# Optimization experiments

Measured on AMD Instinct MI355X. Metric: run time of the kernel, lower is better.

## Reference

```python
import jax, jax.numpy as jnp
import numpy as np

B, S, D, H = 2, 2048, 1024, 16
DK = D // H
ROPE_BASE = 10000.0


def setup_inputs() -> dict:
    key = jax.random.key(0)
    ks = jax.random.split(key, 6)
    x = jax.random.normal(ks[0], (B, S, D), dtype=jnp.float32)
    # causal mask, broadcastable to [B,H,S,S]; masked_fill where mask==0
    mask = jnp.tril(jnp.ones((S, S), dtype=bool))[None, None]
    position_ids = jnp.tile(jnp.arange(S, dtype=jnp.int32)[None, :], (B, 1))
    sc = 1.0 / np.sqrt(D)
    Wq = jax.random.normal(ks[1], (D, D), dtype=jnp.float32) * sc
    Wk = jax.random.normal(ks[2], (D, D), dtype=jnp.float32) * sc
    Wv = jax.random.normal(ks[3], (D, D), dtype=jnp.float32) * sc
    Wo = jax.random.normal(ks[4], (D, D), dtype=jnp.float32) * sc
    bo = jnp.zeros((D,), dtype=jnp.float32)
    return {"x": x, "mask": mask, "position_ids": position_ids,
            "Wq": Wq, "Wk": Wk, "Wv": Wv, "Wo": Wo, "bo": bo}


def _rotate_half(t):
    t1, t2 = t[..., : t.shape[-1] // 2], t[..., t.shape[-1] // 2:]
    return jnp.concatenate((-t2, t1), axis=-1)


def reference(x, mask, position_ids, Wq, Wk, Wv, Wo, bo):
    b, s, d = x.shape
    h, dk = H, DK
    scale = 1.0 / np.sqrt(dk)

    def proj(W):  # torch Linear: x @ W.T -> [b,h,s,dk]
        return (x @ W.T).reshape(b, s, h, dk).transpose(0, 2, 1, 3)

    Q, K, V = proj(Wq), proj(Wk), proj(Wv)

    # rotary tables (computed in fp32, matching RotaryEmbedding)
    inv_freq = 1.0 / (ROPE_BASE ** (jnp.arange(0, dk, 2, dtype=jnp.float32) / dk))
    t = jnp.arange(s, dtype=jnp.float32)
    freqs = jnp.outer(t, inv_freq)            # [s, dk/2]
    emb = jnp.concatenate((freqs, freqs), -1) # [s, dk]
    cos = jnp.cos(emb)[position_ids][:, None]  # [b,1,s,dk]
    sin = jnp.sin(emb)[position_ids][:, None]
    Q = Q * cos + _rotate_half(Q) * sin
    K = K * cos + _rotate_half(K) * sin

    scores = jnp.einsum('bhqd,bhkd->bhqk', Q, K) * scale
    scores = jnp.where(mask, scores, jnp.float32(-1e9))
    attn = jax.nn.softmax(scores, axis=-1)  # dropout is identity in eval
    out = jnp.einsum('bhqk,bhkd->bhqd', attn, V)
    out = out.transpose(0, 2, 1, 3).reshape(b, s, d)
    return out @ Wo.T + bo
```

## Files before the change

### kernel.cpp

```cpp
#include <hip/hip_runtime.h>
#include <hip/hip_bf16.h>
#include <cstdint>

#define BB 2
#define SS 2048
#define DD 1024
#define HH 16
#define DK 64
#define MROWS (BB*SS)
#define NQKV  (3*DD)

typedef __bf16 bf16x8 __attribute__((ext_vector_type(8)));
typedef float  f32x4  __attribute__((ext_vector_type(4)));
typedef float  f32x16 __attribute__((ext_vector_type(16)));
typedef unsigned u32x2 __attribute__((ext_vector_type(2)));

static __device__ __forceinline__ unsigned short f2bf(float f) {
    __bf16 h = (__bf16)f;
    return __builtin_bit_cast(unsigned short, h);
}
static __device__ __forceinline__ float bf2f(unsigned short u) {
    return (float)__builtin_bit_cast(__bf16, u);
}

#define GLOAD16(gsrc, ldst) \
    __builtin_amdgcn_global_load_lds((const __attribute__((address_space(1))) void*)(gsrc), \
                                     (__attribute__((address_space(3))) void*)(ldst), 16, 0, 0)

static __device__ __forceinline__ void pl32_swap(unsigned &x, unsigned &y) {
#if __has_builtin(__builtin_amdgcn_permlane32_swap)
    u32x2 r = __builtin_amdgcn_permlane32_swap(x, y, false, false);
    x = r[0]; y = r[1];
#else
    asm volatile("v_permlane32_swap_b32 %0, %1" : "+v"(x), "+v"(y));
#endif
}
static __device__ __forceinline__ float swap_half(float v, bool hi) {
    unsigned x = __builtin_bit_cast(unsigned, v), y = x;
    pl32_swap(x, y);
    return __builtin_bit_cast(float, hi ? x : y);
}
template<int BASE> static __device__ __forceinline__ bf16x8 cvt_chunk(const f32x16 &p) {
    unsigned x0, y0, x1, y1;
    asm("v_cvt_pk_bf16_f32 %0, %1, %2" : "=v"(x0) : "v"(p[BASE+0]), "v"(p[BASE+1]));
    asm("v_cvt_pk_bf16_f32 %0, %1, %2" : "=v"(y0) : "v"(p[BASE+4]), "v"(p[BASE+5]));
    asm("v_cvt_pk_bf16_f32 %0, %1, %2" : "=v"(x1) : "v"(p[BASE+2]), "v"(p[BASE+3]));
    asm("v_cvt_pk_bf16_f32 %0, %1, %2" : "=v"(y1) : "v"(p[BASE+6]), "v"(p[BASE+7]));
    pl32_swap(x0, y0);
    pl32_swap(x1, y1);
    union { unsigned u[4]; bf16x8 v; } r;
    r.u[0] = x0; r.u[1] = x1; r.u[2] = y0; r.u[3] = y1;
    return r.v;
}

__global__ void cast_all(const float* __restrict__ x,  const float* __restrict__ wq,
                         const float* __restrict__ wk, const float* __restrict__ wv,
                         const float* __restrict__ wo,
                         unsigned short* __restrict__ xb, unsigned short* __restrict__ wqkv,
                         unsigned short* __restrict__ wob)
{
    const int NX = MROWS * DD;
    const int NW = DD * DD;
    const int total = (NX + 4 * NW) / 8;
    for (int i = blockIdx.x * blockDim.x + threadIdx.x; i < total; i += gridDim.x * blockDim.x) {
        int base = i * 8;
        const float* src; unsigned short* dst; int off;
        if      (base < NX)          { src = x;  dst = xb;          off = base; }
        else if (base < NX + NW)     { src = wq; dst = wqkv;        off = base - NX; }
        else if (base < NX + 2*NW)   { src = wk; dst = wqkv + NW;   off = base - NX - NW; }
        else if (base < NX + 3*NW)   { src = wv; dst = wqkv + 2*NW; off = base - NX - 2*NW; }
        else                         { src = wo; dst = wob;         off = base - NX - 3*NW; }
        float4 a = *(const float4*)(src + off);
        float4 b = *(const float4*)(src + off + 4);
        union { unsigned short s[8]; uint4 v; } u;
        u.s[0] = f2bf(a.x); u.s[1] = f2bf(a.y); u.s[2] = f2bf(a.z); u.s[3] = f2bf(a.w);
        u.s[4] = f2bf(b.x); u.s[5] = f2bf(b.y); u.s[6] = f2bf(b.z); u.s[7] = f2bf(b.w);
        *(uint4*)(dst + off) = u.v;
    }
}

__global__ void rope_table(float* __restrict__ tabc, float* __restrict__ tabs)
{
    int i = blockIdx.x * blockDim.x + threadIdx.x;
    int s = i >> 5, d = i & 31;
    float inv = exp2f(-(float)d * (13.287712379549449f / 32.f));
    float ang = (float)s * inv;
    tabc[i] = cosf(ang);
    tabs[i] = sinf(ang);
}

__global__ __launch_bounds__(512) void gemm_qkv(
    const unsigned short* __restrict__ A, const unsigned short* __restrict__ Bm,
    const int* __restrict__ pids,
    const float* __restrict__ tabc, const float* __restrict__ tabs,
    unsigned short* __restrict__ Qb, unsigned short* __restrict__ Kb,
    unsigned short* __restrict__ Vr)
{
    __shared__ __align__(16) unsigned short sA[2][16384];
    __shared__ __align__(16) unsigned short sB[2][16384];
    const int tid = threadIdx.x;
    const int w = tid >> 6, l = tid & 63;
    const int wm = w >> 2, wn = w & 3;
    const int lr = l & 15, lg = l >> 4;
    const int swz = (blockIdx.x & 7) * 24 + (blockIdx.x >> 3);
    const int bx = swz % 12, by = swz / 12;
    const int mBase = by * 256;
    const int sr  = tid >> 3;
    const int scb = (tid & 7) * 8;
    const int sksw = scb ^ ((sr & 7) * 8);
    const int rdsw = (lr & 7) * 8;

    f32x4 acc[8][4] = {};

    auto stage = [&](int kt, int bb) {
        #pragma unroll
        for (int r = 0; r < 4; ++r) {
            GLOAD16(A  + (size_t)(mBase + r*64 + sr) * DD + kt + sksw,
                    &sA[bb][r*4096 + sr*64 + scb]);
            GLOAD16(Bm + (size_t)(bx*256 + r*64 + sr) * DD + kt + sksw,
                    &sB[bb][r*4096 + sr*64 + scb]);
        }
    };

    stage(0, 0);
    __syncthreads();

    for (int t = 0; t < 16; ++t) {
        const int cur = t & 1;
        #pragma unroll
        for (int p = 0; p < 4; ++p) {
            const int rh = p & 1, ks = p >> 1;
            bf16x8 af[4], bfv[4];
            #pragma unroll
            for (int rf = 0; rf < 4; ++rf) {
                int ra = wm*128 + rh*64 + rf*16 + lr;
                af[rf] = *(const bf16x8*)&sA[cur][ra*64 + ((ks*32 + lg*8) ^ rdsw)];
            }
            #pragma unroll
            for (int cf = 0; cf < 4; ++cf) {
                int rb = wn*64 + cf*16 + lr;
                bfv[cf] = *(const bf16x8*)&sB[cur][rb*64 + ((ks*32 + lg*8) ^ rdsw)];
            }
            if (p == 0 && t < 15) stage((t+1)*64, cur ^ 1);
            __builtin_amdgcn_s_barrier();
            asm volatile("s_waitcnt lgkmcnt(0)" ::: "memory");
            __builtin_amdgcn_sched_barrier(0);
            __builtin_amdgcn_s_setprio(1);
            #pragma unroll
            for (int rf = 0; rf < 4; ++rf)
                #pragma unroll
                for (int cf = 0; cf < 4; ++cf)
                    acc[rh*4+rf][cf] = __builtin_amdgcn_mfma_f32_16x16x32_bf16(
                        af[rf], bfv[cf], acc[rh*4+rf][cf], 0, 0, 0);
            __builtin_amdgcn_s_setprio(0);
            if (p < 3) __builtin_amdgcn_s_barrier();
        }
        __syncthreads();
    }

    if (bx < 8) {
        const bool isQ = bx < 4;
        unsigned short* dst = isQ ? Qb : Kb;
        const float qsc = isQ ? 0.1803368801111244f : 1.0f;
        const int colbase = (bx & 3)*256 + wn*64;
        #pragma unroll
        for (int rr = 0; rr < 8; ++rr) {
            #pragma unroll
            for (int j = 0; j < 4; ++j) {
                int row = mBase + wm*128 + rr*16 + lg*4 + j;
                int pos = pids[row];
                #pragma unroll
                for (int cf = 0; cf < 2; ++cf) {
                    int d = cf*16 + lr;
                    float cc = tabc[pos*32 + d];
                    float sn = tabs[pos*32 + d];
                    float a  = acc[rr][cf][j];
                    float bb2 = acc[rr][cf+2][j];
                    dst[(size_t)row * DD + colbase + d]      = f2bf((a*cc - bb2*sn) * qsc);
                    dst[(size_t)row * DD + colbase + d + 32] = f2bf((bb2*cc + a*sn) * qsc);
                }
            }
        }
    } else {
        const int colbase = (bx - 8)*256 + wn*64;
        #pragma unroll
        for (int rr = 0; rr < 8; ++rr) {
            #pragma unroll
            for (int j = 0; j < 4; ++j) {
                int row = mBase + wm*128 + rr*16 + lg*4 + j;
                #pragma unroll
                for (int cf = 0; cf < 4; ++cf)
                    Vr[(size_t)row * DD + colbase + cf*16 + lr] = f2bf(acc[rr][cf][j]);
            }
        }
    }
}

__global__ __launch_bounds__(256) void gemm_bt(
    const unsigned short* __restrict__ A, const unsigned short* __restrict__ Bm,
    float* __restrict__ Cout, const float* __restrict__ bias,
    int M, int N, int K)
{
    __shared__ __align__(16) unsigned short sA[2][128 * 64];
    __shared__ __align__(16) unsigned short sB[2][128 * 64];
    const int tid = threadIdx.x;
    const int w = tid >> 6, l = tid & 63;
    const int wm = w >> 1, wn = w & 1;
    const int lr = l & 15, lg = l >> 4;
    const int nwg = gridDim.x;
    const int cpx = nwg >> 3;
    const int swz = (blockIdx.x & 7) * cpx + (blockIdx.x >> 3);
    const int nbx = N >> 7;
    const int bx = swz % nbx, by = swz / nbx;
    const int mBase = by * 128, nBase = bx * 128;
    const int srow = tid >> 3;
    const int skof = (tid & 7) * 8;

    f32x4 acc[4][4] = {};

    #pragma unroll
    for (int i = 0; i < 4; ++i) {
        GLOAD16(A  + (size_t)(mBase + i*32 + srow) * K + skof, &sA[0][i*2048 + w*512]);
        GLOAD16(Bm + (size_t)(nBase + i*32 + srow) * K + skof, &sB[0][i*2048 + w*512]);
    }
    int cur = 0;

    for (int kt = 0; kt < K; kt += 64) {
        __syncthreads();
        if (kt + 64 < K) {
            #pragma unroll
            for (int i = 0; i < 4; ++i) {
                GLOAD16(A  + (size_t)(mBase + i*32 + srow) * K + kt + 64 + skof, &sA[cur^1][i*2048 + w*512]);
                GLOAD16(Bm + (size_t)(nBase + i*32 + srow) * K + kt + 64 + skof, &sB[cur^1][i*2048 + w*512]);
            }
        }
        #pragma unroll
        for (int kk = 0; kk < 2; ++kk) {
            bf16x8 af[4], bfv[4];
            #pragma unroll
            for (int mi = 0; mi < 4; ++mi)
                af[mi] = *(const bf16x8*)&sA[cur][(wm*64 + mi*16 + lr)*64 + kk*32 + lg*8];
            #pragma unroll
            for (int ni = 0; ni < 4; ++ni)
                bfv[ni] = *(const bf16x8*)&sB[cur][(wn*64 + ni*16 + lr)*64 + kk*32 + lg*8];
            #pragma unroll
            for (int mi = 0; mi < 4; ++mi)
                #pragma unroll
                for (int ni = 0; ni < 4; ++ni)
                    acc[mi][ni] = __builtin_amdgcn_mfma_f32_16x16x32_bf16(af[mi], bfv[ni], acc[mi][ni], 0, 0, 0);
        }
        cur ^= 1;
    }
    #pragma unroll
    for (int mi = 0; mi < 4; ++mi) {
        #pragma unroll
        for (int j = 0; j < 4; ++j) {
            int row = mBase + wm*64 + mi*16 + lg*4 + j;
            #pragma unroll
            for (int ni = 0; ni < 4; ++ni) {
                int col = nBase + wn*64 + ni*16 + lr;
                Cout[(size_t)row * N + col] = acc[mi][ni][j] + bias[col];
            }
        }
    }
}

__global__ __launch_bounds__(256) void v_transpose(
    const unsigned short* __restrict__ Vr, unsigned short* __restrict__ Vt)
{
    __shared__ __align__(16) unsigned short sT[64 * 64];
    const int bh = blockIdx.y;
    const int st = blockIdx.x;
    const int b = bh >> 4, h = bh & 15;
    const int tid = threadIdx.x;
    #pragma unroll
    for (int i = 0; i < 2; ++i) {
        int c = tid + i*256;
        int s = c >> 3, cb = c & 7;
        const unsigned short* src = Vr + (size_t)(b*SS + st*64 + s) * DD + h*64 + cb*8;
        uint4 v = *(const uint4*)src;
        *(uint4*)&sT[s*64 + ((cb ^ (s >> 3)) * 8)] = v;
    }
    __syncthreads();
    #pragma unroll
    for (int i = 0; i < 2; ++i) {
        int c = tid + i*256;
        int d = c >> 3, sb = c & 7;
        union { unsigned short u[8]; uint4 v; } o;
        #pragma unroll
        for (int e = 0; e < 8; ++e) {
            int s = sb*8 + e;
            o.u[e] = sT[s*64 + (((d >> 3) ^ (s >> 3)) * 8) + (d & 7)];
        }
        *(uint4*)(Vt + (size_t)(bh*64 + d) * SS + st*64 + sb*8) = o.v;
    }
}

__global__ __launch_bounds__(256, 2) void attn_fwd(
    const unsigned short* __restrict__ Qb,
    const unsigned short* __restrict__ Kb,
    const unsigned short* __restrict__ Vt,
    unsigned short* __restrict__ Ob)
{
    __shared__ __align__(16) unsigned short sK[2][64 * 64];
    __shared__ __align__(16) unsigned short sV[2][64 * 64];
    const int tid = threadIdx.x;
    const int w = tid >> 6, l = tid & 63;
    const int lq = l & 31;
    const int hi5 = l >> 5;
    const bool hb = hi5 != 0;

    const int xcd  = blockIdx.x & 7;
    const int c    = blockIdx.x >> 3;
    const int gsel = c & 3;
    const int t    = c >> 2;
    const int qt   = (t < 8) ? t : 23 - t;
    const int bh   = xcd * 4 + gsel;
    const int b = bh >> 4, h = bh & 15;

    const int srow = tid >> 3;
    const int skof = (tid & 7) * 8;
    const int sksw = skof ^ ((srow & 7) * 8);
    const int sw   = (lq & 7) * 8;
    const float THR = 12.0f;

    const unsigned kR0 = (unsigned)((b*SS + srow) * DD + h*64 + sksw);
    const unsigned kR1 = kR0 + (unsigned)(32 * DD);
    const unsigned vR0 = (unsigned)((bh*64 + srow) * SS + sksw);
    const unsigned vR1 = vR0 + (unsigned)(32 * SS);

    bf16x8 qf[4];
    {
        const unsigned short* qp = Qb + (size_t)(b*SS + qt*128 + w*32 + lq) * DD + h*64 + hi5*8;
        #pragma unroll
        for (int dkc = 0; dkc < 4; ++dkc)
            qf[dkc] = *(const bf16x8*)(qp + dkc*16);
    }
    const int q_lane = qt*128 + w*32 + lq;
    const int wbase  = qt*128 + w*32;
    const int total  = 2*qt + 2;

    f32x16 o0 = {}, o1 = {};
    float mrow = -3.0e38f, lsum = 0.f;
    int cur = 0;

    GLOAD16(Kb + kR0, &sK[0][w*512]);
    GLOAD16(Kb + kR1, &sK[0][2048 + w*512]);
    GLOAD16(Vt + vR0, &sV[0][w*512]);
    GLOAD16(Vt + vR1, &sV[0][2048 + w*512]);

    for (int kt = 0; kt < total; ++kt) {
        __syncthreads();
        if (kt + 1 < total) {
            unsigned ko = (unsigned)(kt + 1) << 16;
            unsigned vo = (unsigned)(kt + 1) << 6;
            GLOAD16(Kb + kR0 + ko, &sK[cur^1][w*512]);
            GLOAD16(Kb + kR1 + ko, &sK[cur^1][2048 + w*512]);
            GLOAD16(Vt + vR0 + vo, &sV[cur^1][w*512]);
            GLOAD16(Vt + vR1 + vo, &sV[cur^1][2048 + w*512]);
        }

        f32x16 p0 = {}, p1 = {};
        __builtin_amdgcn_s_setprio(1);
        #pragma unroll
        for (int dkc = 0; dkc < 4; ++dkc) {
            bf16x8 k0 = *(const bf16x8*)&sK[cur][lq*64 + ((dkc*16 + hi5*8) ^ sw)];
            p0 = __builtin_amdgcn_mfma_f32_32x32x16_bf16(k0, qf[dkc], p0, 0, 0, 0);
        }
        #pragma unroll
        for (int dkc = 0; dkc < 4; ++dkc) {
            bf16x8 k1 = *(const bf16x8*)&sK[cur][(32 + lq)*64 + ((dkc*16 + hi5*8) ^ sw)];
            p1 = __builtin_amdgcn_mfma_f32_32x32x16_bf16(k1, qf[dkc], p1, 0, 0, 0);
        }
        __builtin_amdgcn_s_setprio(0);

        if (kt*64 + 63 > wbase) {
            const int kb0 = kt*64 + 4*hi5;
            #pragma unroll
            for (int r = 0; r < 16; ++r) {
                const int cr = (r & 3) + 8*(r >> 2);
                if (kb0 + cr > q_lane)      p0[r] = -1e30f;
                if (kb0 + 32 + cr > q_lane) p1[r] = -1e30f;
            }
        }

        float tt[16];
        #pragma unroll
        for (int r = 0; r < 16; ++r) tt[r] = fmaxf(p0[r], p1[r]);
        #pragma unroll
        for (int s2 = 8; s2 >= 1; s2 >>= 1)
            #pragma unroll
            for (int r = 0; r < 8; ++r)
                if (r < s2) tt[r] = fmaxf(tt[r], tt[r + s2]);
        float tmx = fmaxf(tt[0], swap_half(tt[0], hb));

        float growth = tmx - mrow;
        if (!__all(growth <= THR)) {
            float mnew = fmaxf(mrow, tmx);
            float alpha = exp2f(mrow - mnew);
            lsum *= alpha;
            mrow = mnew;
            #pragma unroll
            for (int r = 0; r < 16; ++r) { o0[r] *= alpha; o1[r] *= alpha; }
        }

        #pragma unroll
        for (int r = 0; r < 16; ++r) {
            p0[r] = exp2f(p0[r] - mrow);
            p1[r] = exp2f(p1[r] - mrow);
        }
        float st[16];
        #pragma unroll
        for (int r = 0; r < 16; ++r) st[r] = p0[r] + p1[r];
        #pragma unroll
        for (int s2 = 8; s2 >= 1; s2 >>= 1)
            #pragma unroll
            for (int r = 0; r < 8; ++r)
                if (r < s2) st[r] += st[r + s2];
        lsum += st[0];

        __builtin_amdgcn_s_setprio(1);
        {
            bf16x8 pa, vf;
            pa = cvt_chunk<0>(p0);
            vf = *(const bf16x8*)&sV[cur][lq*64 + ((0*16 + hi5*8) ^ sw)];
            o0 = __builtin_amdgcn_mfma_f32_32x32x16_bf16(vf, pa, o0, 0, 0, 0);
            vf = *(const bf16x8*)&sV[cur][(32 + lq)*64 + ((0*16 + hi5*8) ^ sw)];
            o1 = __builtin_amdgcn_mfma_f32_32x32x16_bf16(vf, pa, o1, 0, 0, 0);
            pa = cvt_chunk<8>(p0);
            vf = *(const bf16x8*)&sV[cur][lq*64 + ((1*16 + hi5*8) ^ sw)];
            o0 = __builtin_amdgcn_mfma_f32_32x32x16_bf16(vf, pa, o0, 0, 0, 0);
            vf = *(const bf16x8*)&sV[cur][(32 + lq)*64 + ((1*16 + hi5*8) ^ sw)];
            o1 = __builtin_amdgcn_mfma_f32_32x32x16_bf16(vf, pa, o1, 0, 0, 0);
            pa = cvt_chunk<0>(p1);
            vf = *(const bf16x8*)&sV[cur][lq*64 + ((2*16 + hi5*8) ^ sw)];
            o0 = __builtin_amdgcn_mfma_f32_32x32x16_bf16(vf, pa, o0, 0, 0, 0);
            vf = *(const bf16x8*)&sV[cur][(32 + lq)*64 + ((2*16 + hi5*8) ^ sw)];
            o1 = __builtin_amdgcn_mfma_f32_32x32x16_bf16(vf, pa, o1, 0, 0, 0);
            pa = cvt_chunk<8>(p1);
            vf = *(const bf16x8*)&sV[cur][lq*64 + ((3*16 + hi5*8) ^ sw)];
            o0 = __builtin_amdgcn_mfma_f32_32x32x16_bf16(vf, pa, o0, 0, 0, 0);
            vf = *(const bf16x8*)&sV[cur][(32 + lq)*64 + ((3*16 + hi5*8) ^ sw)];
            o1 = __builtin_amdgcn_mfma_f32_32x32x16_bf16(vf, pa, o1, 0, 0, 0);
        }
        __builtin_amdgcn_s_setprio(0);
        cur ^= 1;
    }

    __syncthreads();
    float ls = lsum + swap_half(lsum, hb);
    float inv = 1.f / ls;
    unsigned short* sO = &sK[0][0] + w * 2048;

    #pragma unroll
    for (int g2 = 0; g2 < 4; ++g2) {
        unsigned ua, ub; uint2 t2;
        float v0 = o0[g2*4+0]*inv, v1 = o0[g2*4+1]*inv, v2 = o0[g2*4+2]*inv, v3 = o0[g2*4+3]*inv;
        asm("v_cvt_pk_bf16_f32 %0, %1, %2" : "=v"(ua) : "v"(v0), "v"(v1));
        asm("v_cvt_pk_bf16_f32 %0, %1, %2" : "=v"(ub) : "v"(v2), "v"(v3));
        t2.x = ua; t2.y = ub;
        *(uint2*)&sO[lq*64 + g2*8 + hi5*4] = t2;
        float w0 = o1[g2*4+0]*inv, w1 = o1[g2*4+1]*inv, w2 = o1[g2*4+2]*inv, w3 = o1[g2*4+3]*inv;
        asm("v_cvt_pk_bf16_f32 %0, %1, %2" : "=v"(ua) : "v"(w0), "v"(w1));
        asm("v_cvt_pk_bf16_f32 %0, %1, %2" : "=v"(ub) : "v"(w2), "v"(w3));
        t2.x = ua; t2.y = ub;
        *(uint2*)&sO[lq*64 + 32 + g2*8 + hi5*4] = t2;
    }
    asm volatile("s_waitcnt lgkmcnt(0)" ::: "memory");
    __builtin_amdgcn_sched_barrier(0);

    const int row = l >> 1, cb2 = (l & 1) * 32;
    const unsigned short* sOr = sO + row*64 + cb2;
    unsigned short* gp = Ob + (size_t)(b*SS + qt*128 + w*32 + row) * DD + h*64 + cb2;
    #pragma unroll
    for (int c2 = 0; c2 < 4; ++c2)
        *(uint4*)(gp + c2*8) = *(const uint4*)(sOr + c2*8);
}

extern "C" void kernel_launch(void* const* d_in, const int* in_sizes, int n_in,
                              void* d_out, int out_size, void* d_ws, size_t ws_size,
                              hipStream_t stream)
{
    const float* x  = (const float*)d_in[0];
    const int* pids = (const int*)d_in[2];
    const float* wq = (const float*)d_in[3];
    const float* wk = (const float*)d_in[4];
    const float* wv = (const float*)d_in[5];
    const float* wo = (const float*)d_in[6];
    const float* bo = (const float*)d_in[7];
    float* out = (float*)d_out;

    char* ws = (char*)d_ws;
    unsigned short* xb   = (unsigned short*)(ws);
    unsigned short* wqkv = (unsigned short*)(ws + (size_t)( 8u<<20));
    unsigned short* wob  = (unsigned short*)(ws + (size_t)(14u<<20));
    unsigned short* Vr   = (unsigned short*)(ws + (size_t)(16u<<20));
    unsigned short* Qb   = (unsigned short*)(ws + (size_t)(40u<<20));
    unsigned short* Kb   = (unsigned short*)(ws + (size_t)(48u<<20));
    unsigned short* Vt   = (unsigned short*)(ws + (size_t)(56u<<20));
    float* tabc          = (float*)(ws + (size_t)(64u<<20));
    float* tabs          = (float*)(ws + (size_t)(64u<<20) + (256u<<10));
    unsigned short* Ob   = xb;

    cast_all<<<dim3(4096), dim3(256), 0, stream>>>(x, wq, wk, wv, wo, xb, wqkv, wob);
    rope_table<<<dim3(256), dim3(256), 0, stream>>>(tabc, tabs);
    gemm_qkv<<<dim3(192), dim3(512), 0, stream>>>(
        xb, wqkv, pids, tabc, tabs, Qb, Kb, Vr);
    v_transpose<<<dim3(32, 32), dim3(256), 0, stream>>>(Vr, Vt);
    attn_fwd<<<dim3(512), dim3(256), 0, stream>>>(Qb, Kb, Vt, Ob);
    gemm_bt<<<dim3(256), dim3(256), 0, stream>>>(
        Ob, wob, out, bo, MROWS, DD, DD);
}
```

Before: 137.9 us.

## Load K and V fragments directly from global memory, dropping LDS staging

The attention kernel no longer stages K and V tiles through double-buffered shared memory with async global-to-LDS copies and per-iteration barriers. Each wave now loads its MFMA operand fragments for K and V straight from global memory into registers, and shared memory is kept only for the output transpose. This removes the barriers and LDS traffic, but the four waves now fetch the same K/V tiles redundantly. There is also no software prefetch, so global load latency sits directly in front of the MFMAs.

New measurement: 150.6 us. 9.2% more time.

```diff
diff --git a/kernel.cpp b/kernel.cpp
--- a/kernel.cpp
+++ b/kernel.cpp
@@ -302,8 +302,7 @@
     const unsigned short* __restrict__ Vt,
     unsigned short* __restrict__ Ob)
 {
-    __shared__ __align__(16) unsigned short sK[2][64 * 64];
-    __shared__ __align__(16) unsigned short sV[2][64 * 64];
+    __shared__ __align__(16) unsigned short sO[4][32 * 64];
     const int tid = threadIdx.x;
     const int w = tid >> 6, l = tid & 63;
     const int lq = l & 31;
@@ -317,17 +316,7 @@
     const int qt   = (t < 8) ? t : 23 - t;
     const int bh   = xcd * 4 + gsel;
     const int b = bh >> 4, h = bh & 15;
-
-    const int srow = tid >> 3;
-    const int skof = (tid & 7) * 8;
-    const int sksw = skof ^ ((srow & 7) * 8);
-    const int sw   = (lq & 7) * 8;
     const float THR = 12.0f;
-
-    const unsigned kR0 = (unsigned)((b*SS + srow) * DD + h*64 + sksw);
-    const unsigned kR1 = kR0 + (unsigned)(32 * DD);
-    const unsigned vR0 = (unsigned)((bh*64 + srow) * SS + sksw);
-    const unsigned vR1 = vR0 + (unsigned)(32 * SS);
 
     bf16x8 qf[4];
     {
@@ -340,38 +329,34 @@
     const int wbase  = qt*128 + w*32;
     const int total  = 2*qt + 2;
 
+    const unsigned short* Kp = Kb + (size_t)(b*SS + lq) * DD + h*64 + hi5*8;
+    const unsigned short* Vp = Vt + (size_t)(bh*64 + lq) * SS + hi5*8;
+
     f32x16 o0 = {}, o1 = {};
     float mrow = -3.0e38f, lsum = 0.f;
-    int cur = 0;
-
-    GLOAD16(Kb + kR0, &sK[0][w*512]);
-    GLOAD16(Kb + kR1, &sK[0][2048 + w*512]);
-    GLOAD16(Vt + vR0, &sV[0][w*512]);
-    GLOAD16(Vt + vR1, &sV[0][2048 + w*512]);
 
     for (int kt = 0; kt < total; ++kt) {
-        __syncthreads();
-        if (kt + 1 < total) {
-            unsigned ko = (unsigned)(kt + 1) << 16;
-            unsigned vo = (unsigned)(kt + 1) << 6;
-            GLOAD16(Kb + kR0 + ko, &sK[cur^1][w*512]);
-            GLOAD16(Kb + kR1 + ko, &sK[cur^1][2048 + w*512]);
-            GLOAD16(Vt + vR0 + vo, &sV[cur^1][w*512]);
-            GLOAD16(Vt + vR1 + vo, &sV[cur^1][2048 + w*512]);
+        const unsigned short* kp0 = Kp + (size_t)(kt*64) * DD;
+        const unsigned short* kp1 = kp0 + 32*DD;
+        const unsigned short* vp0 = Vp + kt*64;
+        const unsigned short* vp1 = vp0 + (size_t)32*SS;
+        bf16x8 k0f[4], k1f[4], v0f[4], v1f[4];
+        #pragma unroll
+        for (int dkc = 0; dkc < 4; ++dkc) {
+            k0f[dkc] = *(const bf16x8*)(kp0 + dkc*16);
+            k1f[dkc] = *(const bf16x8*)(kp1 + dkc*16);
+            v0f[dkc] = *(const bf16x8*)(vp0 + dkc*16);
+            v1f[dkc] = *(const bf16x8*)(vp1 + dkc*16);
         }
 
         f32x16 p0 = {}, p1 = {};
         __builtin_amdgcn_s_setprio(1);
         #pragma unroll
-        for (int dkc = 0; dkc < 4; ++dkc) {
-            bf16x8 k0 = *(const bf16x8*)&sK[cur][lq*64 + ((dkc*16 + hi5*8) ^ sw)];
-            p0 = __builtin_amdgcn_mfma_f32_32x32x16_bf16(k0, qf[dkc], p0, 0, 0, 0);
-        }
-        #pragma unroll
-        for (int dkc = 0; dkc < 4; ++dkc) {
-            bf16x8 k1 = *(const bf16x8*)&sK[cur][(32 + lq)*64 + ((dkc*16 + hi5*8) ^ sw)];
-            p1 = __builtin_amdgcn_mfma_f32_32x32x16_bf16(k1, qf[dkc], p1, 0, 0, 0);
-        }
+        for (int dkc = 0; dkc < 4; ++dkc)
+            p0 = __builtin_amdgcn_mfma_f32_32x32x16_bf16(k0f[dkc], qf[dkc], p0, 0, 0, 0);
+        #pragma unroll
+        for (int dkc = 0; dkc < 4; ++dkc)
+            p1 = __builtin_amdgcn_mfma_f32_32x32x16_bf16(k1f[dkc], qf[dkc], p1, 0, 0, 0);
         __builtin_amdgcn_s_setprio(0);
 
         if (kt*64 + 63 > wbase) {
@@ -421,36 +406,26 @@
 
         __builtin_amdgcn_s_setprio(1);
         {
-            bf16x8 pa, vf;
+            bf16x8 pa;
             pa = cvt_chunk<0>(p0);
-            vf = *(const bf16x8*)&sV[cur][lq*64 + ((0*16 + hi5*8) ^ sw)];
-            o0 = __builtin_amdgcn_mfma_f32_32x32x16_bf16(vf, pa, o0, 0, 0, 0);
-            vf = *(const bf16x8*)&sV[cur][(32 + lq)*64 + ((0*16 + hi5*8) ^ sw)];
-            o1 = __builtin_amdgcn_mfma_f32_32x32x16_bf16(vf, pa, o1, 0, 0, 0);
+            o0 = __builtin_amdgcn_mfma_f32_32x32x16_bf16(v0f[0], pa, o0, 0, 0, 0);
+            o1 = __builtin_amdgcn_mfma_f32_32x32x16_bf16(v1f[0], pa, o1, 0, 0, 0);
             pa = cvt_chunk<8>(p0);
-            vf = *(const bf16x8*)&sV[cur][lq*64 + ((1*16 + hi5*8) ^ sw)];
-            o0 = __builtin_amdgcn_mfma_f32_32x32x16_bf16(vf, pa, o0, 0, 0, 0);
-            vf = *(const bf16x8*)&sV[cur][(32 + lq)*64 + ((1*16 + hi5*8) ^ sw)];
-            o1 = __builtin_amdgcn_mfma_f32_32x32x16_bf16(vf, pa, o1, 0, 0, 0);
+            o0 = __builtin_amdgcn_mfma_f32_32x32x16_bf16(v0f[1], pa, o0, 0, 0, 0);
+            o1 = __builtin_amdgcn_mfma_f32_32x32x16_bf16(v1f[1], pa, o1, 0, 0, 0);
             pa = cvt_chunk<0>(p1);
-            vf = *(const bf16x8*)&sV[cur][lq*64 + ((2*16 + hi5*8) ^ sw)];
-            o0 = __builtin_amdgcn_mfma_f32_32x32x16_bf16(vf, pa, o0, 0, 0, 0);
-            vf = *(const bf16x8*)&sV[cur][(32 + lq)*64 + ((2*16 + hi5*8) ^ sw)];
-            o1 = __builtin_amdgcn_mfma_f32_32x32x16_bf16(vf, pa, o1, 0, 0, 0);
+            o0 = __builtin_amdgcn_mfma_f32_32x32x16_bf16(v0f[2], pa, o0, 0, 0, 0);
+            o1 = __builtin_amdgcn_mfma_f32_32x32x16_bf16(v1f[2], pa, o1, 0, 0, 0);
             pa = cvt_chunk<8>(p1);
-            vf = *(const bf16x8*)&sV[cur][lq*64 + ((3*16 + hi5*8) ^ sw)];
-            o0 = __builtin_amdgcn_mfma_f32_32x32x16_bf16(vf, pa, o0, 0, 0, 0);
-            vf = *(const bf16x8*)&sV[cur][(32 + lq)*64 + ((3*16 + hi5*8) ^ sw)];
-            o1 = __builtin_amdgcn_mfma_f32_32x32x16_bf16(vf, pa, o1, 0, 0, 0);
+            o0 = __builtin_amdgcn_mfma_f32_32x32x16_bf16(v0f[3], pa, o0, 0, 0, 0);
+            o1 = __builtin_amdgcn_mfma_f32_32x32x16_bf16(v1f[3], pa, o1, 0, 0, 0);
         }
         __builtin_amdgcn_s_setprio(0);
-        cur ^= 1;
-    }
-
-    __syncthreads();
+    }
+
     float ls = lsum + swap_half(lsum, hb);
     float inv = 1.f / ls;
-    unsigned short* sO = &sK[0][0] + w * 2048;
+    unsigned short* sOw = &sO[w][0];
 
     #pragma unroll
     for (int g2 = 0; g2 < 4; ++g2) {
@@ -459,18 +434,18 @@
         asm("v_cvt_pk_bf16_f32 %0, %1, %2" : "=v"(ua) : "v"(v0), "v"(v1));
         asm("v_cvt_pk_bf16_f32 %0, %1, %2" : "=v"(ub) : "v"(v2), "v"(v3));
         t2.x = ua; t2.y = ub;
-        *(uint2*)&sO[lq*64 + g2*8 + hi5*4] = t2;
+        *(uint2*)&sOw[lq*64 + g2*8 + hi5*4] = t2;
         float w0 = o1[g2*4+0]*inv, w1 = o1[g2*4+1]*inv, w2 = o1[g2*4+2]*inv, w3 = o1[g2*4+3]*inv;
         asm("v_cvt_pk_bf16_f32 %0, %1, %2" : "=v"(ua) : "v"(w0), "v"(w1));
         asm("v_cvt_pk_bf16_f32 %0, %1, %2" : "=v"(ub) : "v"(w2), "v"(w3));
         t2.x = ua; t2.y = ub;
-        *(uint2*)&sO[lq*64 + 32 + g2*8 + hi5*4] = t2;
+        *(uint2*)&sOw[lq*64 + 32 + g2*8 + hi5*4] = t2;
     }
     asm volatile("s_waitcnt lgkmcnt(0)" ::: "memory");
     __builtin_amdgcn_sched_barrier(0);
 
     const int row = l >> 1, cb2 = (l & 1) * 32;
-    const unsigned short* sOr = sO + row*64 + cb2;
+    const unsigned short* sOr = sOw + row*64 + cb2;
     unsigned short* gp = Ob + (size_t)(b*SS + qt*128 + w*32 + row) * DD + h*64 + cb2;
     #pragma unroll
     for (int c2 = 0; c2 < 4; ++c2)
```

## Split attention KV range in two halves with separate merge kernel

Applied to the files above, without the earlier changes.

Attention work is split across twice as many blocks: each (head, q-tile) processes half of its causal key range and writes unnormalized fp32 partial outputs plus row max and sum. A new merge kernel rescales and combines the two halves into bf16. Launch bounds are raised to allow more blocks per CU. An explicit LDS wait and sched barrier are also dropped from the QKV GEMM inner loop. The trade is extra fp32 partial traffic and an extra launch in exchange for better load balance and occupancy.

Measured after the change: 135.1 us. 2.1% less time.

```diff
diff --git a/kernel.cpp b/kernel.cpp
--- a/kernel.cpp
+++ b/kernel.cpp
@@ -143,8 +143,6 @@
             }
             if (p == 0 && t < 15) stage((t+1)*64, cur ^ 1);
             __builtin_amdgcn_s_barrier();
-            asm volatile("s_waitcnt lgkmcnt(0)" ::: "memory");
-            __builtin_amdgcn_sched_barrier(0);
             __builtin_amdgcn_s_setprio(1);
             #pragma unroll
             for (int rf = 0; rf < 4; ++rf)
@@ -296,14 +294,16 @@
     }
 }
 
-__global__ __launch_bounds__(256, 2) void attn_fwd(
+__global__ __launch_bounds__(256, 4) void attn_fwd(
     const unsigned short* __restrict__ Qb,
     const unsigned short* __restrict__ Kb,
     const unsigned short* __restrict__ Vt,
-    unsigned short* __restrict__ Ob)
-{
-    __shared__ __align__(16) unsigned short sK[2][64 * 64];
-    __shared__ __align__(16) unsigned short sV[2][64 * 64];
+    float* __restrict__ OpA,
+    float* __restrict__ OpB,
+    float* __restrict__ Ml)
+{
+    __shared__ __align__(16) unsigned short sK[2][4096];
+    __shared__ __align__(16) unsigned short sV[2][4096];
     const int tid = threadIdx.x;
     const int w = tid >> 6, l = tid & 63;
     const int lq = l & 31;
@@ -312,9 +312,10 @@
 
     const int xcd  = blockIdx.x & 7;
     const int c    = blockIdx.x >> 3;
-    const int gsel = c & 3;
-    const int t    = c >> 2;
-    const int qt   = (t < 8) ? t : 23 - t;
+    const int gsel = (c >> 1) & 3;
+    const int half = c & 1;
+    const int t2   = c >> 3;
+    const int qt   = (t2 < 8) ? t2 : 23 - t2;
     const int bh   = xcd * 4 + gsel;
     const int b = bh >> 4, h = bh & 15;
 
@@ -324,11 +325,6 @@
     const int sw   = (lq & 7) * 8;
     const float THR = 12.0f;
 
-    const unsigned kR0 = (unsigned)((b*SS + srow) * DD + h*64 + sksw);
-    const unsigned kR1 = kR0 + (unsigned)(32 * DD);
-    const unsigned vR0 = (unsigned)((bh*64 + srow) * SS + sksw);
-    const unsigned vR1 = vR0 + (unsigned)(32 * SS);
-
     bf16x8 qf[4];
     {
         const unsigned short* qp = Qb + (size_t)(b*SS + qt*128 + w*32 + lq) * DD + h*64 + hi5*8;
@@ -338,27 +334,29 @@
     }
     const int q_lane = qt*128 + w*32 + lq;
     const int wbase  = qt*128 + w*32;
-    const int total  = 2*qt + 2;
+    const int kt0    = half * (qt + 1);
+    const int nsub   = qt + 1;
 
     f32x16 o0 = {}, o1 = {};
     float mrow = -3.0e38f, lsum = 0.f;
     int cur = 0;
 
-    GLOAD16(Kb + kR0, &sK[0][w*512]);
-    GLOAD16(Kb + kR1, &sK[0][2048 + w*512]);
-    GLOAD16(Vt + vR0, &sV[0][w*512]);
-    GLOAD16(Vt + vR1, &sV[0][2048 + w*512]);
-
-    for (int kt = 0; kt < total; ++kt) {
+    auto stage = [&](int kt, int bb) {
+        #pragma unroll
+        for (int r = 0; r < 2; ++r) {
+            GLOAD16(Kb + (size_t)(b*SS + kt*64 + r*32 + srow) * DD + h*64 + sksw,
+                    &sK[bb][r*2048 + w*512]);
+            GLOAD16(Vt + (size_t)(bh*64 + r*32 + srow) * SS + kt*64 + sksw,
+                    &sV[bb][r*2048 + w*512]);
+        }
+    };
+
+    stage(kt0, 0);
+
+    for (int s = 0; s < nsub; ++s) {
+        const int kt = kt0 + s;
         __syncthreads();
-        if (kt + 1 < total) {
-            unsigned ko = (unsigned)(kt + 1) << 16;
-            unsigned vo = (unsigned)(kt + 1) << 6;
-            GLOAD16(Kb + kR0 + ko, &sK[cur^1][w*512]);
-            GLOAD16(Kb + kR1 + ko, &sK[cur^1][2048 + w*512]);
-            GLOAD16(Vt + vR0 + vo, &sV[cur^1][w*512]);
-            GLOAD16(Vt + vR1 + vo, &sV[cur^1][2048 + w*512]);
-        }
+        if (s + 1 < nsub) stage(kt + 1, cur ^ 1);
 
         f32x16 p0 = {}, p1 = {};
         __builtin_amdgcn_s_setprio(1);
@@ -369,7 +367,7 @@
         }
         #pragma unroll
         for (int dkc = 0; dkc < 4; ++dkc) {
-            bf16x8 k1 = *(const bf16x8*)&sK[cur][(32 + lq)*64 + ((dkc*16 + hi5*8) ^ sw)];
+            bf16x8 k1 = *(const bf16x8*)&sK[cur][2048 + lq*64 + ((dkc*16 + hi5*8) ^ sw)];
             p1 = __builtin_amdgcn_mfma_f32_32x32x16_bf16(k1, qf[dkc], p1, 0, 0, 0);
         }
         __builtin_amdgcn_s_setprio(0);
@@ -421,27 +419,27 @@
 
         __builtin_amdgcn_s_setprio(1);
         {
-            bf16x8 pa, vf;
-            pa = cvt_chunk<0>(p0);
+            bf16x8 pv, vf;
+            pv = cvt_chunk<0>(p0);
             vf = *(const bf16x8*)&sV[cur][lq*64 + ((0*16 + hi5*8) ^ sw)];
-            o0 = __builtin_amdgcn_mfma_f32_32x32x16_bf16(vf, pa, o0, 0, 0, 0);
-            vf = *(const bf16x8*)&sV[cur][(32 + lq)*64 + ((0*16 + hi5*8) ^ sw)];
-            o1 = __builtin_amdgcn_mfma_f32_32x32x16_bf16(vf, pa, o1, 0, 0, 0);
-            pa = cvt_chunk<8>(p0);
+            o0 = __builtin_amdgcn_mfma_f32_32x32x16_bf16(vf, pv, o0, 0, 0, 0);
+            vf = *(const bf16x8*)&sV[cur][2048 + lq*64 + ((0*16 + hi5*8) ^ sw)];
+            o1 = __builtin_amdgcn_mfma_f32_32x32x16_bf16(vf, pv, o1, 0, 0, 0);
+            pv = cvt_chunk<8>(p0);
             vf = *(const bf16x8*)&sV[cur][lq*64 + ((1*16 + hi5*8) ^ sw)];
-            o0 = __builtin_amdgcn_mfma_f32_32x32x16_bf16(vf, pa, o0, 0, 0, 0);
-            vf = *(const bf16x8*)&sV[cur][(32 + lq)*64 + ((1*16 + hi5*8) ^ sw)];
-            o1 = __builtin_amdgcn_mfma_f32_32x32x16_bf16(vf, pa, o1, 0, 0, 0);
-            pa = cvt_chunk<0>(p1);
+            o0 = __builtin_amdgcn_mfma_f32_32x32x16_bf16(vf, pv, o0, 0, 0, 0);
+            vf = *(const bf16x8*)&sV[cur][2048 + lq*64 + ((1*16 + hi5*8) ^ sw)];
+            o1 = __builtin_amdgcn_mfma_f32_32x32x16_bf16(vf, pv, o1, 0, 0, 0);
+            pv = cvt_chunk<0>(p1);
             vf = *(const bf16x8*)&sV[cur][lq*64 + ((2*16 + hi5*8) ^ sw)];
-            o0 = __builtin_amdgcn_mfma_f32_32x32x16_bf16(vf, pa, o0, 0, 0, 0);
-            vf = *(const bf16x8*)&sV[cur][(32 + lq)*64 + ((2*16 + hi5*8) ^ sw)];
-            o1 = __builtin_amdgcn_mfma_f32_32x32x16_bf16(vf, pa, o1, 0, 0, 0);
-            pa = cvt_chunk<8>(p1);
+            o0 = __builtin_amdgcn_mfma_f32_32x32x16_bf16(vf, pv, o0, 0, 0, 0);
+            vf = *(const bf16x8*)&sV[cur][2048 + lq*64 + ((2*16 + hi5*8) ^ sw)];
+            o1 = __builtin_amdgcn_mfma_f32_32x32x16_bf16(vf, pv, o1, 0, 0, 0);
+            pv = cvt_chunk<8>(p1);
             vf = *(const bf16x8*)&sV[cur][lq*64 + ((3*16 + hi5*8) ^ sw)];
-            o0 = __builtin_amdgcn_mfma_f32_32x32x16_bf16(vf, pa, o0, 0, 0, 0);
-            vf = *(const bf16x8*)&sV[cur][(32 + lq)*64 + ((3*16 + hi5*8) ^ sw)];
-            o1 = __builtin_amdgcn_mfma_f32_32x32x16_bf16(vf, pa, o1, 0, 0, 0);
+            o0 = __builtin_amdgcn_mfma_f32_32x32x16_bf16(vf, pv, o0, 0, 0, 0);
+            vf = *(const bf16x8*)&sV[cur][2048 + lq*64 + ((3*16 + hi5*8) ^ sw)];
+            o1 = __builtin_amdgcn_mfma_f32_32x32x16_bf16(vf, pv, o1, 0, 0, 0);
         }
         __builtin_amdgcn_s_setprio(0);
         cur ^= 1;
@@ -449,32 +447,60 @@
 
     __syncthreads();
     float ls = lsum + swap_half(lsum, hb);
-    float inv = 1.f / ls;
-    unsigned short* sO = &sK[0][0] + w * 2048;
+    float* sOf = (w < 2) ? (float*)&sK[w][0] : (float*)&sV[w - 2][0];
 
     #pragma unroll
     for (int g2 = 0; g2 < 4; ++g2) {
-        unsigned ua, ub; uint2 t2;
-        float v0 = o0[g2*4+0]*inv, v1 = o0[g2*4+1]*inv, v2 = o0[g2*4+2]*inv, v3 = o0[g2*4+3]*inv;
-        asm("v_cvt_pk_bf16_f32 %0, %1, %2" : "=v"(ua) : "v"(v0), "v"(v1));
-        asm("v_cvt_pk_bf16_f32 %0, %1, %2" : "=v"(ub) : "v"(v2), "v"(v3));
-        t2.x = ua; t2.y = ub;
-        *(uint2*)&sO[lq*64 + g2*8 + hi5*4] = t2;
-        float w0 = o1[g2*4+0]*inv, w1 = o1[g2*4+1]*inv, w2 = o1[g2*4+2]*inv, w3 = o1[g2*4+3]*inv;
-        asm("v_cvt_pk_bf16_f32 %0, %1, %2" : "=v"(ua) : "v"(w0), "v"(w1));
-        asm("v_cvt_pk_bf16_f32 %0, %1, %2" : "=v"(ub) : "v"(w2), "v"(w3));
-        t2.x = ua; t2.y = ub;
-        *(uint2*)&sO[lq*64 + 32 + g2*8 + hi5*4] = t2;
+        f32x4 t0, t1;
+        #pragma unroll
+        for (int j = 0; j < 4; ++j) { t0[j] = o0[g2*4 + j]; t1[j] = o1[g2*4 + j]; }
+        *(f32x4*)&sOf[lq*64 + g2*8 + hi5*4]      = t0;
+        *(f32x4*)&sOf[lq*64 + 32 + g2*8 + hi5*4] = t1;
     }
     asm volatile("s_waitcnt lgkmcnt(0)" ::: "memory");
     __builtin_amdgcn_sched_barrier(0);
 
+    float* Op = half ? OpB : OpA;
     const int row = l >> 1, cb2 = (l & 1) * 32;
-    const unsigned short* sOr = sO + row*64 + cb2;
-    unsigned short* gp = Ob + (size_t)(b*SS + qt*128 + w*32 + row) * DD + h*64 + cb2;
-    #pragma unroll
-    for (int c2 = 0; c2 < 4; ++c2)
-        *(uint4*)(gp + c2*8) = *(const uint4*)(sOr + c2*8);
+    const float* sOr = sOf + row*64 + cb2;
+    float* gp = Op + (size_t)(b*SS + qt*128 + w*32 + row) * DD + h*64 + cb2;
+    #pragma unroll
+    for (int c2 = 0; c2 < 8; ++c2)
+        *(f32x4*)(gp + c2*4) = *(const f32x4*)(sOr + c2*4);
+
+    if (!hb) {
+        int qrow = qt*128 + w*32 + lq;
+        float* mlp = Ml + (((size_t)half*32 + bh)*2048 + qrow)*2;
+        mlp[0] = mrow;
+        mlp[1] = ls;
+    }
+}
+
+__global__ __launch_bounds__(256) void attn_merge(
+    const float* __restrict__ OpA, const float* __restrict__ OpB,
+    const float* __restrict__ Ml, unsigned short* __restrict__ Ob)
+{
+    int e = blockIdx.x * 256 + threadIdx.x;
+    int row = e >> 8;
+    int col = (e & 255) * 4;
+    int b = row >> 11, q = row & 2047;
+    int h = col >> 6;
+    int bh = b*16 + h;
+    const float* mlA = Ml + ((size_t)bh*2048 + q)*2;
+    const float* mlB = Ml + (((size_t)32 + bh)*2048 + q)*2;
+    float mA = mlA[0], lA = mlA[1];
+    float mB = mlB[0], lB = mlB[1];
+    float m  = fmaxf(mA, mB);
+    float sA = exp2f(mA - m), sB = exp2f(mB - m);
+    float linv = 1.f / (lA*sA + lB*sB);
+    float fa = sA * linv, fb = sB * linv;
+    f32x4 a = *(const f32x4*)(OpA + (size_t)e*4);
+    f32x4 bq = *(const f32x4*)(OpB + (size_t)e*4);
+    union { unsigned short s[4]; uint2 v; } o;
+    #pragma unroll
+    for (int j = 0; j < 4; ++j)
+        o.s[j] = f2bf(a[j]*fa + bq[j]*fb);
+    *(uint2*)(Ob + (size_t)e*4) = o.v;
 }
 
 extern "C" void kernel_launch(void* const* d_in, const int* in_sizes, int n_in,
@@ -495,11 +521,14 @@
     unsigned short* wqkv = (unsigned short*)(ws + (size_t)( 8u<<20));
     unsigned short* wob  = (unsigned short*)(ws + (size_t)(14u<<20));
     unsigned short* Vr   = (unsigned short*)(ws + (size_t)(16u<<20));
+    float* Ml            = (float*)(ws + (size_t)(16u<<20));
+    float* OpA           = (float*)(ws + (size_t)(24u<<20));
     unsigned short* Qb   = (unsigned short*)(ws + (size_t)(40u<<20));
     unsigned short* Kb   = (unsigned short*)(ws + (size_t)(48u<<20));
     unsigned short* Vt   = (unsigned short*)(ws + (size_t)(56u<<20));
     float* tabc          = (float*)(ws + (size_t)(64u<<20));
     float* tabs          = (float*)(ws + (size_t)(64u<<20) + (256u<<10));
+    float* OpB           = out;
     unsigned short* Ob   = xb;
 
     cast_all<<<dim3(4096), dim3(256), 0, stream>>>(x, wq, wk, wv, wo, xb, wqkv, wob);
@@ -507,7 +536,8 @@
     gemm_qkv<<<dim3(192), dim3(512), 0, stream>>>(
         xb, wqkv, pids, tabc, tabs, Qb, Kb, Vr);
     v_transpose<<<dim3(32, 32), dim3(256), 0, stream>>>(Vr, Vt);
-    attn_fwd<<<dim3(512), dim3(256), 0, stream>>>(Qb, Kb, Vt, Ob);
+    attn_fwd<<<dim3(1024), dim3(256), 0, stream>>>(Qb, Kb, Vt, OpA, OpB, Ml);
+    attn_merge<<<dim3(4096), dim3(256), 0, stream>>>(OpA, OpB, Ml, Ob);
     gemm_bt<<<dim3(256), dim3(256), 0, stream>>>(
         Ob, wob, out, bo, MROWS, DD, DD);
 }
```
